# Kernel optimization log

Measured on AMD Instinct MI355X. Metric: run time of the kernel, lower is better.

Reference implementation:

```python
import jax, jax.numpy as jnp
import numpy as np


def _sum_matrix():
    # [69, 42] mask matrix reproducing compute_sums exactly (incl. bugs):
    # feature k = sum over cells where M[k] == 1, board flattened row-major (6x7).
    M = np.zeros((69, 42), dtype=np.float32)
    m = M.reshape(69, 6, 7)
    # 24 row window sums
    for row in range(6):
        for i in range(4):
            m[row * 4 + i, row, i:i + 4] = 1.0
    # 21 column window sums
    for col in range(7):
        for i in range(3):
            m[24 + col * 3 + i, i:i + 4, col] = 1.0
    # 12 'upward diag' sums: source sums the FULL 4x4 block of the row-flipped
    # board, i.e. original rows (2-off)..(5-off), cols col..col+3.
    for off in range(3):
        for col in range(4):
            m[45 + off * 4 + col, 2 - off:6 - off, col:col + 4] = 1.0
    # 12 'downward diag' sums: allocated but never written in source -> zeros.
    return jnp.asarray(M)


_M = _sum_matrix()  # [69, 42]


def setup_inputs() -> dict:
    key = jax.random.key(0)
    k1, k2, k3 = jax.random.split(key, 3)
    B = 524288
    game_state = jax.random.normal(k1, (B, 42), dtype=jnp.float32)
    W = jax.random.normal(k2, (7, 111), dtype=jnp.float32) * (1.0 / np.sqrt(111.0))
    b = jax.random.normal(k3, (7,), dtype=jnp.float32) * 0.01
    return {"game_state": game_state, "W": W, "b": b}


def reference(game_state, W, b):
    # sums: [B, 69] = all windowed sums as one GEMM against the mask matrix
    sums = game_state @ _M.T
    feats = jnp.concatenate([game_state, sums], axis=1)  # [B, 111]
    return feats @ W.T + b  # [B, 7]
```

## Files before the change

### kernel.cpp

```cpp
#include <hip/hip_runtime.h>


#define ROW_PAD 43

__global__ __launch_bounds__(320)
void ddqn_weff(const float* __restrict__ W, float* __restrict__ weff) {
    int tid = threadIdx.x;
    if (tid >= 7 * 42) return;
    int j = tid / 42;
    int d = tid % 42;
    float acc = W[j * 111 + d];
    int r = d / 7, c = d % 7;
    const float* ws = W + j * 111 + 42;
    for (int i = 0; i < 4; ++i)
        if (c >= i && c <= i + 3) acc += ws[r * 4 + i];
    for (int i = 0; i < 3; ++i)
        if (r >= i && r <= i + 3) acc += ws[24 + c * 3 + i];
    for (int off = 0; off < 3; ++off)
        for (int col = 0; col < 4; ++col)
            if (r >= 2 - off && r <= 5 - off && c >= col && c <= col + 3)
                acc += ws[45 + off * 4 + col];
    weff[j * 42 + d] = acc;
}

__global__ __launch_bounds__(256)
void ddqn_main(const float* __restrict__ gs,
               const float* __restrict__ weff,
               const float* __restrict__ b,
               float* __restrict__ out) {
    __shared__ float wl[7 * 44 + 8];
    __shared__ float tile[4][64 * ROW_PAD];

    const int t = threadIdx.x;
    for (int i = t; i < 7 * 44; i += 256) {
        int j = i / 44, d = i % 44;
        wl[i] = (d < 42) ? weff[j * 42 + d] : 0.0f;
    }
    if (t < 7) wl[7 * 44 + t] = b[t];
    __syncthreads();

    const int w = t >> 6;
    const int l = t & 63;
    float* tw = tile[w];

    const size_t tileIdx = (size_t)blockIdx.x * 4 + w;
    const float* src = gs + tileIdx * (64 * 42);

    int row = l / 42;
    int col = l - row * 42;
    #pragma unroll
    for (int k = 0; k < 42; ++k) {
        tw[row * ROW_PAD + col] = src[k * 64 + l];
        row += 1; col += 22;
        if (col >= 42) { col -= 42; row += 1; }
    }
    __builtin_amdgcn_wave_barrier();

    float acc[7];
    #pragma unroll
    for (int j = 0; j < 7; ++j) acc[j] = wl[7 * 44 + j];

    const float* xrow = tw + l * ROW_PAD;
    const float4* wl4 = (const float4*)wl;
    #pragma unroll
    for (int dq = 0; dq < 44; dq += 4) {
        float x0 = xrow[dq];
        float x1 = xrow[dq + 1];
        float x2 = (dq + 2 < 42) ? xrow[dq + 2] : 0.0f;
        float x3 = (dq + 3 < 42) ? xrow[dq + 3] : 0.0f;
        #pragma unroll
        for (int j = 0; j < 7; ++j) {
            const float4 wv = wl4[j * 11 + (dq >> 2)];
            acc[j] = fmaf(x0, wv.x, acc[j]);
            acc[j] = fmaf(x1, wv.y, acc[j]);
            acc[j] = fmaf(x2, wv.z, acc[j]);
            acc[j] = fmaf(x3, wv.w, acc[j]);
        }
    }

    float* o = out + (tileIdx * 64 + l) * 7;
    #pragma unroll
    for (int j = 0; j < 7; ++j) o[j] = acc[j];
}

extern "C" void kernel_launch(void* const* d_in, const int* in_sizes, int n_in,
                              void* d_out, int out_size, void* d_ws, size_t ws_size,
                              hipStream_t stream) {
    const float* gs = (const float*)d_in[0];
    const float* W  = (const float*)d_in[1];
    const float* b  = (const float*)d_in[2];
    float* out  = (float*)d_out;
    float* weff = (float*)d_ws;

    ddqn_weff<<<dim3(1), dim3(320), 0, stream>>>(W, weff);

    int B = in_sizes[0] / 42;
    int tiles = B / 64;
    ddqn_main<<<dim3(tiles / 4), dim3(256), 0, stream>>>(gs, weff, b, out);
}
```

Measured before the change: 143.2 us.

## Fuse effective-weight precompute into main kernel and coalesce output stores via LDS

Drops the separate single-block launch that folded the window-sum mask into effective weights. Each block now recomputes the 7x42 effective weights from W in shared memory after staging its input tile, which removes one launch and the dependency between the two kernels. Outputs are first written to an LDS buffer and then stored to global memory in contiguous 64-wide chunks rather than 7 strided floats per thread. The cost is redundant weight computation in every block and extra LDS use.

Measured after the change: 151.3 us. 1.06x slower.

```diff
diff --git a/kernel.cpp b/kernel.cpp
--- a/kernel.cpp
+++ b/kernel.cpp
@@ -3,42 +3,17 @@
 
 #define ROW_PAD 43
 
-__global__ __launch_bounds__(320)
-void ddqn_weff(const float* __restrict__ W, float* __restrict__ weff) {
-    int tid = threadIdx.x;
-    if (tid >= 7 * 42) return;
-    int j = tid / 42;
-    int d = tid % 42;
-    float acc = W[j * 111 + d];
-    int r = d / 7, c = d % 7;
-    const float* ws = W + j * 111 + 42;
-    for (int i = 0; i < 4; ++i)
-        if (c >= i && c <= i + 3) acc += ws[r * 4 + i];
-    for (int i = 0; i < 3; ++i)
-        if (r >= i && r <= i + 3) acc += ws[24 + c * 3 + i];
-    for (int off = 0; off < 3; ++off)
-        for (int col = 0; col < 4; ++col)
-            if (r >= 2 - off && r <= 5 - off && c >= col && c <= col + 3)
-                acc += ws[45 + off * 4 + col];
-    weff[j * 42 + d] = acc;
-}
-
 __global__ __launch_bounds__(256)
-void ddqn_main(const float* __restrict__ gs,
-               const float* __restrict__ weff,
-               const float* __restrict__ b,
-               float* __restrict__ out) {
-    __shared__ float wl[7 * 44 + 8];
+void ddqn_fused(const float* __restrict__ gs,
+                const float* __restrict__ W,
+                const float* __restrict__ b,
+                float* __restrict__ out) {
+    __shared__ float wl[7 * 44];
+    __shared__ float bl[7];
     __shared__ float tile[4][64 * ROW_PAD];
+    __shared__ float obuf[4][64 * 7];
 
     const int t = threadIdx.x;
-    for (int i = t; i < 7 * 44; i += 256) {
-        int j = i / 44, d = i % 44;
-        wl[i] = (d < 42) ? weff[j * 42 + d] : 0.0f;
-    }
-    if (t < 7) wl[7 * 44 + t] = b[t];
-    __syncthreads();
-
     const int w = t >> 6;
     const int l = t & 63;
     float* tw = tile[w];
@@ -46,19 +21,45 @@
     const size_t tileIdx = (size_t)blockIdx.x * 4 + w;
     const float* src = gs + tileIdx * (64 * 42);
 
-    int row = l / 42;
-    int col = l - row * 42;
-    #pragma unroll
-    for (int k = 0; k < 42; ++k) {
-        tw[row * ROW_PAD + col] = src[k * 64 + l];
-        row += 1; col += 22;
-        if (col >= 42) { col -= 42; row += 1; }
+    {
+        int row = l / 42;
+        int col = l - row * 42;
+        #pragma unroll
+        for (int k = 0; k < 42; ++k) {
+            tw[row * ROW_PAD + col] = src[k * 64 + l];
+            row += 1; col += 22;
+            if (col >= 42) { col -= 42; row += 1; }
+        }
     }
-    __builtin_amdgcn_wave_barrier();
+
+    for (int i = t; i < 7 * 44; i += 256) {
+        int j = i / 44, d = i - j * 44;
+        float acc = 0.0f;
+        if (d < 42) {
+            acc = W[j * 111 + d];
+            int r = d / 7, c = d - r * 7;
+            const float* ws = W + j * 111 + 42;
+            #pragma unroll
+            for (int i4 = 0; i4 < 4; ++i4)
+                if (c >= i4 && c <= i4 + 3) acc += ws[r * 4 + i4];
+            #pragma unroll
+            for (int i3 = 0; i3 < 3; ++i3)
+                if (r >= i3 && r <= i3 + 3) acc += ws[24 + c * 3 + i3];
+            #pragma unroll
+            for (int off = 0; off < 3; ++off)
+                #pragma unroll
+                for (int col4 = 0; col4 < 4; ++col4)
+                    if (r >= 2 - off && r <= 5 - off && c >= col4 && c <= col4 + 3)
+                        acc += ws[45 + off * 4 + col4];
+        }
+        wl[i] = acc;
+    }
+    if (t < 7) bl[t] = b[t];
+    __syncthreads();
 
     float acc[7];
     #pragma unroll
-    for (int j = 0; j < 7; ++j) acc[j] = wl[7 * 44 + j];
+    for (int j = 0; j < 7; ++j) acc[j] = bl[j];
 
     const float* xrow = tw + l * ROW_PAD;
     const float4* wl4 = (const float4*)wl;
@@ -78,9 +79,13 @@
         }
     }
 
-    float* o = out + (tileIdx * 64 + l) * 7;
+    float* ob = obuf[w];
     #pragma unroll
-    for (int j = 0; j < 7; ++j) o[j] = acc[j];
+    for (int j = 0; j < 7; ++j) ob[l * 7 + j] = acc[j];
+    __builtin_amdgcn_wave_barrier();
+    float* o = out + tileIdx * 448;
+    #pragma unroll
+    for (int k = 0; k < 7; ++k) o[k * 64 + l] = ob[k * 64 + l];
 }
 
 extern "C" void kernel_launch(void* const* d_in, const int* in_sizes, int n_in,
@@ -89,12 +94,9 @@
     const float* gs = (const float*)d_in[0];
     const float* W  = (const float*)d_in[1];
     const float* b  = (const float*)d_in[2];
-    float* out  = (float*)d_out;
-    float* weff = (float*)d_ws;
-
-    ddqn_weff<<<dim3(1), dim3(320), 0, stream>>>(W, weff);
+    float* out = (float*)d_out;
 
     int B = in_sizes[0] / 42;
     int tiles = B / 64;
-    ddqn_main<<<dim3(tiles / 4), dim3(256), 0, stream>>>(gs, weff, b, out);
+    ddqn_fused<<<dim3(tiles / 4), dim3(256), 0, stream>>>(gs, W, b, out);
 }
```
